# Kernel optimization log

Measured on AMD Instinct MI355X. Metric: run time of the kernel, lower is better.

## Reference

```python
import jax, jax.numpy as jnp
import numpy as np

NUM_PREFIXES = 64  # == head_dim in this config


def setup_inputs() -> dict:
    key = jax.random.key(0)
    ks = jax.random.split(key, 12)
    B, S, H = 2, 2048, 1024
    hd = NUM_PREFIXES
    nh = H // hd              # 16 heads
    din = dout = 128
    kg = H // dout            # key conv groups = 8
    P = S + hd                # position_dim = 2112
    f = jnp.float32
    sc = 0.02
    hidden = jax.random.normal(ks[0], (B, S, H), f)
    # one-hot positions: prefix tokens (first hd) use slots [S, S+hd), rest use their index
    idx = jnp.where(jnp.arange(S) < hd, S + jnp.arange(S), jnp.arange(S))
    pos = jnp.broadcast_to(jax.nn.one_hot(idx, P, dtype=f)[None], (B, S, P))
    mask = jnp.ones((B, 1, S, S), f)  # peak_into_future=True -> full visibility
    return {
        "hidden_states": hidden,
        "position_embeddings": pos,
        "attention_mask": mask,
        "Wq_head": sc * jax.random.normal(ks[1], (hd, nh, nh), f),
        "Wk_group": sc * jax.random.normal(ks[2], (kg, din, din), f),
        "Wk_head": sc * jax.random.normal(ks[3], (dout, kg, kg), f),
        "Wv_head": sc * jax.random.normal(ks[4], (hd, nh, nh), f),
        "p_attn": sc * jax.random.normal(ks[5], (3 * hd, P), f),
        "p_expand": sc * jax.random.normal(ks[6], (3, 1, nh), f),
        "Wc": sc * jax.random.normal(ks[7], (hd, nh, nh), f),
        "Wg": sc * jax.random.normal(ks[8], (2, H), f),
        "Ug": sc * jax.random.normal(ks[9], (2, H), f),
        "Vg": sc * jax.random.normal(ks[10], (2, P), f),
        "bg": jnp.zeros((2,), f),
    }


def reference(hidden_states, position_embeddings, attention_mask,
              Wq_head, Wk_group, Wk_head, Wv_head,
              p_attn, p_expand, Wc, Wg, Ug, Vg, bg):
    B, S, H = hidden_states.shape
    hd, nh, _ = Wq_head.shape
    kg, din, _ = Wk_group.shape
    npf = NUM_PREFIXES
    # LinearDescent.forward: zero out prefix-prefix attention block
    mask = attention_mask.at[:, :, :npf, :npf].set(0.0)
    # --- Attention: conv2d/per-dim head-mixing projections (proj_conv2d, proj_transpose) ---
    xh = hidden_states.reshape(B, S, nh, hd)
    q = jnp.einsum('bshd,dhg->bsgd', xh, Wq_head)      # per-dim mixing across heads
    v = jnp.einsum('bshd,dhg->bsgd', xh, Wv_head)
    # key path: per-group linear (kg groups of din), then per-dim mixing across groups
    xg = hidden_states.reshape(B, S, kg, din)
    k1 = jnp.einsum('bsgd,gde->bsge', xg, Wk_group)
    k2 = jnp.einsum('bsgd,dgh->bshd', k1, Wk_head)     # (B,S,kg,dout)
    k = k2.reshape(B, S, nh, hd)
    # positional q/k/v via p_attn (3*hd x P) + per-head expansion via p_expand (3,1,nh)
    pqkv = jnp.einsum('bsp,cp->bsc', position_embeddings, p_attn).reshape(B, S, 3, hd)
    q = q + p_expand[0, 0][None, None, :, None] * pqkv[:, :, 0][:, :, None, :]
    k = k + p_expand[1, 0][None, None, :, None] * pqkv[:, :, 1][:, :, None, :]
    v = v + p_expand[2, 0][None, None, :, None] * pqkv[:, :, 2][:, :, None, :]
    # linear (non-softmax) attention with multiplicative mask, no causal mask
    scores = jnp.einsum('bqhd,bkhd->bhqk', q, k) * mask
    ctx = jnp.einsum('bhqk,bkhd->bqhd', scores, v)
    out = jnp.einsum('bqhd,dhg->bqgd', ctx, Wc).reshape(B, S, H)
    # --- Gates: two sigmoid gates from hidden, attention output, and positions ---
    g = jax.nn.sigmoid(hidden_states @ Wg.T + out @ Ug.T + position_embeddings @ Vg.T + bg)
    return g[..., 0:1] * out + g[..., 1:2] * hidden_states
```

## Files before the change

### kernel.cpp

```cpp
#include <hip/hip_runtime.h>
#include <math.h>

#define SS   2048
#define PP   2112
#define C3   192
#define NZCAP 16

__device__ __forceinline__ void fma4s(float4& a, float s, const float4& b) {
    a.x += s*b.x; a.y += s*b.y; a.z += s*b.z; a.w += s*b.w;
}
__device__ __forceinline__ void fme4(float4& a, const float4& x, const float4& w) {
    a.x += x.x*w.x; a.y += x.y*w.y; a.z += x.z*w.z; a.w += x.w*w.w;
}
__device__ __forceinline__ float comp(const float4& v, int j) {
    return j==0 ? v.x : j==1 ? v.y : j==2 ? v.z : v.w;
}

__global__ __launch_bounds__(256) void k0_prep(
    const float* __restrict__ Wq, const float* __restrict__ Wv,
    const float* __restrict__ Wc, const float* __restrict__ Wkh,
    const float* __restrict__ Wkg, const float* __restrict__ p_attn,
    float* __restrict__ WqT, float* __restrict__ WvT, float* __restrict__ WcT,
    float* __restrict__ WkhT, float* __restrict__ WkgT, float* __restrict__ pT)
{
    const int t = threadIdx.x, blk = blockIdx.x;
    if (blk < 48) {
        const float* src = (blk < 16) ? Wq : (blk < 32) ? Wv : Wc;
        float* dst = (blk < 16) ? WqT : (blk < 32) ? WvT : WcT;
        int base = (blk & 15) * 1024;
        #pragma unroll
        for (int i = 0; i < 4; ++i) {
            int didx = base + i*256 + t;
            int d = didx & 63, g = (didx>>6)&15, h = didx>>10;
            dst[didx] = src[(d<<8)+(h<<4)+g];
        }
    } else if (blk < 56) {
        int base = (blk-48)*1024;
        #pragma unroll
        for (int i = 0; i < 4; ++i) {
            int didx = base + i*256 + t;
            int dk = didx&127, hk = (didx>>7)&7, g = didx>>10;
            WkhT[didx] = Wkh[dk*64 + g*8 + hk];
        }
    } else if (blk < 184) {
        int base = (blk-56)*1024;
        #pragma unroll
        for (int i = 0; i < 4; ++i) {
            int didx = base + i*256 + t;
            int e = didx&127, g = (didx>>7)&7, d = didx>>10;
            WkgT[didx] = Wkg[(g*128+d)*128 + e];
        }
    } else {
        int base = (blk-184)*1024;
        #pragma unroll
        for (int i = 0; i < 4; ++i) {
            int sidx = base + i*256 + t;
            int c = sidx / PP, p = sidx - c*PP;
            pT[p*C3 + c] = p_attn[sidx];
        }
    }
}

__global__ __launch_bounds__(256) void ka_proj(
    const float* __restrict__ hidden, const float* __restrict__ pos,
    const float* __restrict__ WkgT, const float* __restrict__ WkhT,
    const float* __restrict__ WvT,  const float* __restrict__ pT,
    const float* __restrict__ p_exp, const float* __restrict__ Vg,
    float* __restrict__ ko, float* __restrict__ vo,
    float* __restrict__ pq0, float* __restrict__ posg)
{
    __shared__ __align__(16) float xs[8][1024];
    __shared__ __align__(16) float k1s[8][1024];
    __shared__ __align__(16) float pq[8][C3+4];
    __shared__ int   cnt[8];
    __shared__ int   plist[8][NZCAP];
    __shared__ float vlist[8][NZCAP];

    const int t = threadIdx.x;
    const int row0 = blockIdx.x * 8;

    #pragma unroll
    for (int i = 0; i < 8; ++i)
        ((float4*)xs)[i*256+t] = ((const float4*)hidden)[(size_t)row0*256 + i*256 + t];
    for (int i = t; i < 8*(C3+4); i += 256) ((float*)pq)[i] = 0.f;
    if (t < 8) cnt[t] = 0;
    __syncthreads();

    #pragma unroll
    for (int r = 0; r < 8; ++r) {
        const float4* prow4 = (const float4*)(pos + (size_t)(row0+r)*PP);
        #pragma unroll
        for (int c = 0; c < 3; ++c) {
            int fi = c*256 + t;
            if (fi < PP/4) {
                float4 v4 = prow4[fi];
                float vals[4] = {v4.x, v4.y, v4.z, v4.w};
                #pragma unroll
                for (int u = 0; u < 4; ++u) if (vals[u] != 0.f) {
                    int idx = atomicAdd(&cnt[r], 1);
                    if (idx < NZCAP) { plist[r][idx] = fi*4+u; vlist[r][idx] = vals[u]; }
                    else {
                        int p = fi*4+u; float val = vals[u];
                        for (int cc = 0; cc < C3; ++cc)
                            atomicAdd(&pq[r][cc], val * pT[p*C3+cc]);
                        atomicAdd(&pq[r][C3],   val * Vg[p]);
                        atomicAdd(&pq[r][C3+1], val * Vg[PP+p]);
                    }
                }
            }
        }
    }
    __syncthreads();

    #pragma unroll
    for (int r = 0; r < 8; ++r) {
        int n = min(cnt[r], NZCAP);
        for (int i = 0; i < n; ++i) {
            int p = plist[r][i]; float val = vlist[r][i];
            if (t < C3)           pq[r][t]    += val * pT[p*C3 + t];
            else if (t == C3)     pq[r][C3]   += val * Vg[p];
            else if (t == C3+1)   pq[r][C3+1] += val * Vg[PP+p];
        }
    }
    __syncthreads();

    {
        const int g = t>>4, dq = t&15;
        const float4* WvT4 = (const float4*)WvT;
        const float pev = p_exp[32+g];
        #pragma unroll
        for (int r = 0; r < 8; ++r) {
            float4 av = {0,0,0,0};
            #pragma unroll
            for (int h = 0; h < 16; ++h)
                fme4(av, ((const float4*)xs[r])[h*16+dq], WvT4[(h*16+g)*16+dq]);
            fma4s(av, pev, ((const float4*)&pq[r][128])[dq]);
            ((float4*)vo)[(size_t)(row0+r)*256 + g*16 + dq] = av;
        }
    }

    {
        const int g8 = t>>5, eq = t&31;
        const float4* WkgT4 = (const float4*)WkgT;
        float4 a1[8] = {};
        for (int dq = 0; dq < 32; ++dq) {
            float4 xq[8];
            #pragma unroll
            for (int r = 0; r < 8; ++r) xq[r] = ((const float4*)xs[r])[g8*32 + dq];
            #pragma unroll
            for (int j = 0; j < 4; ++j) {
                int d = dq*4 + j;
                float4 w = WkgT4[(d*8+g8)*32 + eq];
                #pragma unroll
                for (int r = 0; r < 8; ++r) fma4s(a1[r], comp(xq[r], j), w);
            }
        }
        #pragma unroll
        for (int r = 0; r < 8; ++r) ((float4*)k1s[r])[g8*32 + eq] = a1[r];
    }
    __syncthreads();

    {
        const int hk = t>>5, dkq = t&31;
        const int hh = hk*2 + (dkq>>4);
        const float pe = p_exp[16 + hh];
        const float4* WkhT4 = (const float4*)WkhT;
        float4 acc[8] = {};
        #pragma unroll
        for (int g = 0; g < 8; ++g) {
            float4 w = WkhT4[(g*8+hk)*32 + dkq];
            #pragma unroll
            for (int r = 0; r < 8; ++r)
                fme4(acc[r], ((const float4*)k1s[r])[g*32 + dkq], w);
        }
        #pragma unroll
        for (int r = 0; r < 8; ++r) {
            fma4s(acc[r], pe, ((const float4*)&pq[r][64])[dkq&15]);
            ((float4*)ko)[(size_t)(row0+r)*256 + hk*32 + dkq] = acc[r];
        }
    }

    #pragma unroll
    for (int i = 0; i < 2; ++i) {
        int idx = i*256 + t;
        pq0[(size_t)(row0 + (idx>>6))*64 + (idx&63)] = pq[idx>>6][idx&63];
    }
    if (t < 16) posg[(size_t)(row0 + (t>>1))*2 + (t&1)] = pq[t>>1][C3 + (t&1)];
}

__global__ __launch_bounds__(256) void km_kv(
    const float* __restrict__ k, const float* __restrict__ v,
    float* __restrict__ Mpart, float* __restrict__ Mpref)
{
    __shared__ __align__(16) float kt[2048];
    __shared__ __align__(16) float vt[2048];
    const int t  = threadIdx.x;
    const int c  = blockIdx.x >> 5;
    const int bh = blockIdx.x & 31;
    const int b  = bh >> 4, h = bh & 15;
    const int et = t>>4, dt = t&15;
    float acc[4][4]  = {};
    float accp[4][4] = {};

    #pragma unroll
    for (int tile = 0; tile < 4; ++tile) {
        const int r0 = c*128 + tile*32;
        #pragma unroll
        for (int i = 0; i < 2; ++i) {
            int fi = t + 256*i;
            int r = fi>>4, q4 = fi&15;
            size_t ga = (size_t)(b*SS + r0 + r)*256 + h*16 + q4;
            ((float4*)kt)[fi] = ((const float4*)k)[ga];
            ((float4*)vt)[fi] = ((const float4*)v)[ga];
        }
        __syncthreads();
        const bool pf = (c==0) && (tile<2);
        #pragma unroll 4
        for (int r = 0; r < 32; ++r) {
            float4 kk = ((const float4*)kt)[r*16+et];
            float4 vv = ((const float4*)vt)[r*16+dt];
            float ka[4]={kk.x,kk.y,kk.z,kk.w}, va[4]={vv.x,vv.y,vv.z,vv.w};
            #pragma unroll
            for (int i2=0;i2<4;++i2)
                #pragma unroll
                for (int j=0;j<4;++j) acc[i2][j] += ka[i2]*va[j];
            if (pf) {
                #pragma unroll
                for (int i2=0;i2<4;++i2)
                    #pragma unroll
                    for (int j=0;j<4;++j) accp[i2][j] += ka[i2]*va[j];
            }
        }
        __syncthreads();
    }
    float4* Mc = (float4*)(Mpart + ((size_t)c*32 + bh)*4096);
    #pragma unroll
    for (int i2=0;i2<4;++i2) {
        float4 o = {acc[i2][0],acc[i2][1],acc[i2][2],acc[i2][3]};
        Mc[(et*4+i2)*16 + dt] = o;
    }
    if (c == 0) {
        float4* Mp = (float4*)(Mpref + (size_t)bh*4096);
        #pragma unroll
        for (int i2=0;i2<4;++i2) {
            float4 o = {accp[i2][0],accp[i2][1],accp[i2][2],accp[i2][3]};
            Mp[(et*4+i2)*16 + dt] = o;
        }
    }
}

__global__ __launch_bounds__(256) void kr_red(
    const float* __restrict__ Mpart, float* __restrict__ Mfull)
{
    int qid = blockIdx.x*256 + threadIdx.x;
    float4 s = {0,0,0,0};
    #pragma unroll
    for (int c = 0; c < 16; ++c) {
        float4 m = ((const float4*)Mpart)[(size_t)c*32768 + qid];
        s.x+=m.x; s.y+=m.y; s.z+=m.z; s.w+=m.w;
    }
    ((float4*)Mfull)[qid] = s;
}

__global__ __launch_bounds__(256) void kb_out(
    const float* __restrict__ hidden, const float* __restrict__ pq0,
    const float* __restrict__ posg,   const float* __restrict__ Mfull,
    const float* __restrict__ Mpref,  const float* __restrict__ WqT,
    const float* __restrict__ p_exp,  const float* __restrict__ WcT,
    const float* __restrict__ Wg,     const float* __restrict__ Ug,
    const float* __restrict__ bg,     float* __restrict__ yo)
{
    __shared__ __align__(16) float xs[8][1024];
    __shared__ __align__(16) float qs[8][1024];
    __shared__ __align__(16) float pq0s[8][64];
    __shared__ float gs[32];
    const int t  = threadIdx.x;
    const int b  = blockIdx.x >> 8;
    const int s0 = (blockIdx.x & 255) * 8;
    const size_t rqbase = ((size_t)b*SS + s0) * 256;

    float4 xv[8];
    #pragma unroll
    for (int r = 0; r < 8; ++r) {
        xv[r] = ((const float4*)hidden)[rqbase + r*256 + t];
        ((float4*)xs[r])[t] = xv[r];
    }
    if (t < 128) ((float4*)pq0s)[t] = ((const float4*)pq0)[((size_t)b*SS + s0)*16 + t];
    if (t < 32) gs[t] = 0.f;
    __syncthreads();

    float pW0[8], pW1[8];
    {
        float4 w0 = ((const float4*)Wg)[t], w1 = ((const float4*)Wg)[256+t];
        #pragma unroll
        for (int r = 0; r < 8; ++r) {
            pW0[r] = xv[r].x*w0.x + xv[r].y*w0.y + xv[r].z*w0.z + xv[r].w*w0.w;
            pW1[r] = xv[r].x*w1.x + xv[r].y*w1.y + xv[r].z*w1.z + xv[r].w*w1.w;
        }
    }

    const int g = t>>4, dq = t&15;
    {
        const float4* WqT4 = (const float4*)WqT;
        const float peq = p_exp[g];
        #pragma unroll
        for (int r = 0; r < 8; ++r) {
            float4 aq = {0,0,0,0};
            #pragma unroll
            for (int h = 0; h < 16; ++h)
                fme4(aq, ((const float4*)xs[r])[h*16+dq], WqT4[(h*16+g)*16+dq]);
            fma4s(aq, peq, ((const float4*)pq0s[r])[dq]);
            ((float4*)qs[r])[g*16+dq] = aq;
        }
    }
    __syncthreads();

    {
        const float4* Mf4 = (const float4*)Mfull + ((size_t)b*16 + g)*1024;
        const float4* Mp4 = (const float4*)Mpref + ((size_t)b*16 + g)*1024;
        const bool pf = (s0 < 64);
        float4 acc[8] = {};
        for (int eq = 0; eq < 16; ++eq) {
            float4 qq[8];
            #pragma unroll
            for (int r = 0; r < 8; ++r) qq[r] = ((const float4*)qs[r])[g*16 + eq];
            #pragma unroll
            for (int j = 0; j < 4; ++j) {
                int e = eq*4 + j;
                float4 m = Mf4[e*16 + dq];
                if (pf) { float4 mp = Mp4[e*16+dq]; m.x-=mp.x; m.y-=mp.y; m.z-=mp.z; m.w-=mp.w; }
                #pragma unroll
                for (int r = 0; r < 8; ++r) fma4s(acc[r], comp(qq[r],j), m);
            }
        }
        #pragma unroll
        for (int r = 0; r < 8; ++r) ((float4*)xs[r])[g*16 + dq] = acc[r];
    }
    __syncthreads();

    float pU0[8], pU1[8];
    {
        const float4* WcT4 = (const float4*)WcT;
        float4 u0 = ((const float4*)Ug)[g*16+dq], u1 = ((const float4*)Ug)[256 + g*16+dq];
        #pragma unroll
        for (int r = 0; r < 8; ++r) {
            float4 o = {0,0,0,0};
            #pragma unroll
            for (int h = 0; h < 16; ++h)
                fme4(o, ((const float4*)xs[r])[h*16+dq], WcT4[(h*16+g)*16+dq]);
            ((float4*)qs[r])[g*16+dq] = o;
            pU0[r] = o.x*u0.x + o.y*u0.y + o.z*u0.z + o.w*u0.w;
            pU1[r] = o.x*u1.x + o.y*u1.y + o.z*u1.z + o.w*u1.w;
        }
    }

    #pragma unroll
    for (int r = 0; r < 8; ++r) {
        float v0 = pW0[r], v1 = pW1[r], v2 = pU0[r], v3 = pU1[r];
        #pragma unroll
        for (int off = 32; off > 0; off >>= 1) {
            v0 += __shfl_down(v0, off);
            v1 += __shfl_down(v1, off);
            v2 += __shfl_down(v2, off);
            v3 += __shfl_down(v3, off);
        }
        if ((t & 63) == 0) {
            atomicAdd(&gs[r*4+0], v0);
            atomicAdd(&gs[r*4+1], v1);
            atomicAdd(&gs[r*4+2], v2);
            atomicAdd(&gs[r*4+3], v3);
        }
    }
    __syncthreads();

    #pragma unroll
    for (int r = 0; r < 8; ++r) {
        size_t grow = (size_t)b*SS + s0 + r;
        float z0 = gs[r*4+0] + gs[r*4+2] + posg[grow*2+0] + bg[0];
        float z1 = gs[r*4+1] + gs[r*4+3] + posg[grow*2+1] + bg[1];
        float G0 = 1.f/(1.f+expf(-z0));
        float G1 = 1.f/(1.f+expf(-z1));
        float4 o = ((const float4*)qs[r])[t];
        float4 y;
        y.x = G0*o.x + G1*xv[r].x;
        y.y = G0*o.y + G1*xv[r].y;
        y.z = G0*o.z + G1*xv[r].z;
        y.w = G0*o.w + G1*xv[r].w;
        ((float4*)yo)[rqbase + r*256 + t] = y;
    }
}

extern "C" void kernel_launch(void* const* d_in, const int* in_sizes, int n_in,
                              void* d_out, int out_size, void* d_ws, size_t ws_size,
                              hipStream_t stream)
{
    const float* hidden = (const float*)d_in[0];
    const float* pos    = (const float*)d_in[1];
    const float* Wq     = (const float*)d_in[3];
    const float* Wkg    = (const float*)d_in[4];
    const float* Wkh    = (const float*)d_in[5];
    const float* Wv     = (const float*)d_in[6];
    const float* p_attn = (const float*)d_in[7];
    const float* p_exp  = (const float*)d_in[8];
    const float* Wc     = (const float*)d_in[9];
    const float* Wg     = (const float*)d_in[10];
    const float* Ug     = (const float*)d_in[11];
    const float* Vg     = (const float*)d_in[12];
    const float* bg     = (const float*)d_in[13];

    float* ws    = (float*)d_ws;
    float* ko    = ws;
    float* vo    = ws + 4194304;
    float* Mpart = ws + 8388608;
    float* Mpref = ws + 10485760;
    float* Mfull = ws + 10616832;
    float* pq0   = ws + 10747904;
    float* posg  = ws + 11010048;
    float* WqT   = ws + 11018240;
    float* WvT   = ws + 11034624;
    float* WcT   = ws + 11051008;
    float* WkhT  = ws + 11067392;
    float* WkgT  = ws + 11075584;
    float* pT    = ws + 11206656;

    k0_prep<<<dim3(580), dim3(256), 0, stream>>>(Wq, Wv, Wc, Wkh, Wkg, p_attn,
                                                 WqT, WvT, WcT, WkhT, WkgT, pT);
    ka_proj<<<dim3(512), dim3(256), 0, stream>>>(hidden, pos, WkgT, WkhT, WvT, pT,
                                                 p_exp, Vg, ko, vo, pq0, posg);
    km_kv<<<dim3(512), dim3(256), 0, stream>>>(ko, vo, Mpart, Mpref);
    kr_red<<<dim3(128), dim3(256), 0, stream>>>(Mpart, Mfull);
    kb_out<<<dim3(512), dim3(256), 0, stream>>>(hidden, pq0, posg, Mfull, Mpref,
                                                WqT, p_exp, WcT, Wg, Ug, bg, (float*)d_out);
}
```

Measured before the change: 270.1 us.

## Double threads per block in projection/output kernels and split KV chunks finer

```diff
diff --git a/kernel.cpp b/kernel.cpp
--- a/kernel.cpp
+++ b/kernel.cpp
@@ -14,6 +14,9 @@
 }
 __device__ __forceinline__ float comp(const float4& v, int j) {
     return j==0 ? v.x : j==1 ? v.y : j==2 ? v.z : v.w;
+}
+__device__ __forceinline__ float dot4(const float4& a, const float4& b) {
+    return a.x*b.x + a.y*b.y + a.z*b.z + a.w*b.w;
 }
 
 __global__ __launch_bounds__(256) void k0_prep(
@@ -61,7 +64,7 @@
     }
 }
 
-__global__ __launch_bounds__(256) void ka_proj(
+__global__ __launch_bounds__(512) void ka_proj(
     const float* __restrict__ hidden, const float* __restrict__ pos,
     const float* __restrict__ WkgT, const float* __restrict__ WkhT,
     const float* __restrict__ WvT,  const float* __restrict__ pT,
@@ -70,7 +73,6 @@
     float* __restrict__ pq0, float* __restrict__ posg)
 {
     __shared__ __align__(16) float xs[8][1024];
-    __shared__ __align__(16) float k1s[8][1024];
     __shared__ __align__(16) float pq[8][C3+4];
     __shared__ int   cnt[8];
     __shared__ int   plist[8][NZCAP];
@@ -80,9 +82,9 @@
     const int row0 = blockIdx.x * 8;
 
     #pragma unroll
-    for (int i = 0; i < 8; ++i)
-        ((float4*)xs)[i*256+t] = ((const float4*)hidden)[(size_t)row0*256 + i*256 + t];
-    for (int i = t; i < 8*(C3+4); i += 256) ((float*)pq)[i] = 0.f;
+    for (int i = 0; i < 4; ++i)
+        ((float4*)xs)[i*512+t] = ((const float4*)hidden)[(size_t)row0*256 + i*512 + t];
+    for (int i = t; i < 8*(C3+4); i += 512) ((float*)pq)[i] = 0.f;
     if (t < 8) cnt[t] = 0;
     __syncthreads();
 
@@ -90,8 +92,8 @@
     for (int r = 0; r < 8; ++r) {
         const float4* prow4 = (const float4*)(pos + (size_t)(row0+r)*PP);
         #pragma unroll
-        for (int c = 0; c < 3; ++c) {
-            int fi = c*256 + t;
+        for (int c = 0; c < 2; ++c) {
+            int fi = c*512 + t;
             if (fi < PP/4) {
                 float4 v4 = prow4[fi];
                 float vals[4] = {v4.x, v4.y, v4.z, v4.w};
@@ -125,11 +127,12 @@
     __syncthreads();
 
     {
-        const int g = t>>4, dq = t&15;
+        const int rh = t>>8, g = (t>>4)&15, dq = t&15;
         const float4* WvT4 = (const float4*)WvT;
         const float pev = p_exp[32+g];
         #pragma unroll
-        for (int r = 0; r < 8; ++r) {
+        for (int rr = 0; rr < 4; ++rr) {
+            int r = rh*4+rr;
             float4 av = {0,0,0,0};
             #pragma unroll
             for (int h = 0; h < 16; ++h)
@@ -139,52 +142,55 @@
         }
     }
 
-    {
-        const int g8 = t>>5, eq = t&31;
+    float4 a1[4] = {};
+    {
+        const int g8 = t>>6, rh = (t>>5)&1, eq = t&31;
         const float4* WkgT4 = (const float4*)WkgT;
-        float4 a1[8] = {};
         for (int dq = 0; dq < 32; ++dq) {
-            float4 xq[8];
-            #pragma unroll
-            for (int r = 0; r < 8; ++r) xq[r] = ((const float4*)xs[r])[g8*32 + dq];
+            float4 xq[4];
+            #pragma unroll
+            for (int rr = 0; rr < 4; ++rr)
+                xq[rr] = ((const float4*)xs[rh*4+rr])[g8*32 + dq];
             #pragma unroll
             for (int j = 0; j < 4; ++j) {
                 int d = dq*4 + j;
                 float4 w = WkgT4[(d*8+g8)*32 + eq];
                 #pragma unroll
-                for (int r = 0; r < 8; ++r) fma4s(a1[r], comp(xq[r], j), w);
+                for (int rr = 0; rr < 4; ++rr) fma4s(a1[rr], comp(xq[rr], j), w);
             }
         }
-        #pragma unroll
-        for (int r = 0; r < 8; ++r) ((float4*)k1s[r])[g8*32 + eq] = a1[r];
-    }
-    __syncthreads();
-
-    {
-        const int hk = t>>5, dkq = t&31;
+    }
+    __syncthreads();
+    {
+        const int g8 = t>>6, rh = (t>>5)&1, eq = t&31;
+        #pragma unroll
+        for (int rr = 0; rr < 4; ++rr)
+            ((float4*)xs[rh*4+rr])[g8*32 + eq] = a1[rr];
+    }
+    __syncthreads();
+
+    {
+        const int hk = t>>6, rh = (t>>5)&1, dkq = t&31;
         const int hh = hk*2 + (dkq>>4);
         const float pe = p_exp[16 + hh];
         const float4* WkhT4 = (const float4*)WkhT;
-        float4 acc[8] = {};
+        float4 acc[4] = {};
         #pragma unroll
         for (int g = 0; g < 8; ++g) {
             float4 w = WkhT4[(g*8+hk)*32 + dkq];
             #pragma unroll
-            for (int r = 0; r < 8; ++r)
-                fme4(acc[r], ((const float4*)k1s[r])[g*32 + dkq], w);
-        }
-        #pragma unroll
-        for (int r = 0; r < 8; ++r) {
-            fma4s(acc[r], pe, ((const float4*)&pq[r][64])[dkq&15]);
-            ((float4*)ko)[(size_t)(row0+r)*256 + hk*32 + dkq] = acc[r];
-        }
-    }
-
-    #pragma unroll
-    for (int i = 0; i < 2; ++i) {
-        int idx = i*256 + t;
-        pq0[(size_t)(row0 + (idx>>6))*64 + (idx&63)] = pq[idx>>6][idx&63];
-    }
+            for (int rr = 0; rr < 4; ++rr)
+                fme4(acc[rr], ((const float4*)xs[rh*4+rr])[g*32 + dkq], w);
+        }
+        #pragma unroll
+        for (int rr = 0; rr < 4; ++rr) {
+            int r = rh*4+rr;
+            fma4s(acc[rr], pe, ((const float4*)&pq[r][64])[dkq&15]);
+            ((float4*)ko)[(size_t)(row0+r)*256 + hk*32 + dkq] = acc[rr];
+        }
+    }
+
+    pq0[(size_t)(row0 + (t>>6))*64 + (t&63)] = pq[t>>6][t&63];
     if (t < 16) posg[(size_t)(row0 + (t>>1))*2 + (t&1)] = pq[t>>1][C3 + (t&1)];
 }
 
@@ -199,12 +205,13 @@
     const int bh = blockIdx.x & 31;
     const int b  = bh >> 4, h = bh & 15;
     const int et = t>>4, dt = t&15;
+    const bool pf = (c == 0);
     float acc[4][4]  = {};
     float accp[4][4] = {};
 
     #pragma unroll
-    for (int tile = 0; tile < 4; ++tile) {
-        const int r0 = c*128 + tile*32;
+    for (int tile = 0; tile < 2; ++tile) {
+        const int r0 = c*64 + tile*32;
         #pragma unroll
         for (int i = 0; i < 2; ++i) {
             int fi = t + 256*i;
@@ -214,7 +221,6 @@
             ((float4*)vt)[fi] = ((const float4*)v)[ga];
         }
         __syncthreads();
-        const bool pf = (c==0) && (tile<2);
         #pragma unroll 4
         for (int r = 0; r < 32; ++r) {
             float4 kk = ((const float4*)kt)[r*16+et];
@@ -239,7 +245,7 @@
         float4 o = {acc[i2][0],acc[i2][1],acc[i2][2],acc[i2][3]};
         Mc[(et*4+i2)*16 + dt] = o;
     }
-    if (c == 0) {
+    if (pf) {
         float4* Mp = (float4*)(Mpref + (size_t)bh*4096);
         #pragma unroll
         for (int i2=0;i2<4;++i2) {
@@ -253,16 +259,17 @@
     const float* __restrict__ Mpart, float* __restrict__ Mfull)
 {
     int qid = blockIdx.x*256 + threadIdx.x;
+    int bh = qid >> 10, inner = qid & 1023;
     float4 s = {0,0,0,0};
     #pragma unroll
-    for (int c = 0; c < 16; ++c) {
-        float4 m = ((const float4*)Mpart)[(size_t)c*32768 + qid];
+    for (int c = 0; c < 32; ++c) {
+        float4 m = ((const float4*)Mpart)[(((size_t)c*32 + bh)<<10) + inner];
         s.x+=m.x; s.y+=m.y; s.z+=m.z; s.w+=m.w;
     }
     ((float4*)Mfull)[qid] = s;
 }
 
-__global__ __launch_bounds__(256) void kb_out(
+__global__ __launch_bounds__(512) void kb_out(
     const float* __restrict__ hidden, const float* __restrict__ pq0,
     const float* __restrict__ posg,   const float* __restrict__ Mfull,
     const float* __restrict__ Mpref,  const float* __restrict__ WqT,
@@ -279,38 +286,38 @@
     const int s0 = (blockIdx.x & 255) * 8;
     const size_t rqbase = ((size_t)b*SS + s0) * 256;
 
-    float4 xv[8];
-    #pragma unroll
-    for (int r = 0; r < 8; ++r) {
-        xv[r] = ((const float4*)hidden)[rqbase + r*256 + t];
-        ((float4*)xs[r])[t] = xv[r];
-    }
+    #pragma unroll
+    for (int i = 0; i < 4; ++i)
+        ((float4*)xs)[i*512+t] = ((const float4*)hidden)[rqbase + i*512 + t];
     if (t < 128) ((float4*)pq0s)[t] = ((const float4*)pq0)[((size_t)b*SS + s0)*16 + t];
     if (t < 32) gs[t] = 0.f;
     __syncthreads();
 
-    float pW0[8], pW1[8];
-    {
-        float4 w0 = ((const float4*)Wg)[t], w1 = ((const float4*)Wg)[256+t];
-        #pragma unroll
-        for (int r = 0; r < 8; ++r) {
-            pW0[r] = xv[r].x*w0.x + xv[r].y*w0.y + xv[r].z*w0.z + xv[r].w*w0.w;
-            pW1[r] = xv[r].x*w1.x + xv[r].y*w1.y + xv[r].z*w1.z + xv[r].w*w1.w;
-        }
-    }
-
-    const int g = t>>4, dq = t&15;
+    const int rh = t>>8, c = t&255, g = c>>4, dq = c&15;
+
+    float4 xv[4]; float pW0[4], pW1[4];
+    {
+        float4 w0 = ((const float4*)Wg)[c], w1 = ((const float4*)Wg)[256+c];
+        #pragma unroll
+        for (int rr = 0; rr < 4; ++rr) {
+            xv[rr] = ((const float4*)xs[rh*4+rr])[c];
+            pW0[rr] = dot4(xv[rr], w0);
+            pW1[rr] = dot4(xv[rr], w1);
+        }
+    }
+
     {
         const float4* WqT4 = (const float4*)WqT;
         const float peq = p_exp[g];
         #pragma unroll
-        for (int r = 0; r < 8; ++r) {
+        for (int rr = 0; rr < 4; ++rr) {
+            int row = rh*4+rr;
             float4 aq = {0,0,0,0};
             #pragma unroll
             for (int h = 0; h < 16; ++h)
-                fme4(aq, ((const float4*)xs[r])[h*16+dq], WqT4[(h*16+g)*16+dq]);
-            fma4s(aq, peq, ((const float4*)pq0s[r])[dq]);
-            ((float4*)qs[r])[g*16+dq] = aq;
+                fme4(aq, ((const float4*)xs[row])[h*16+dq], WqT4[(h*16+g)*16+dq]);
+            fma4s(aq, peq, ((const float4*)pq0s[row])[dq]);
+            ((float4*)qs[row])[c] = aq;
         }
     }
     __syncthreads();
@@ -319,44 +326,48 @@
         const float4* Mf4 = (const float4*)Mfull + ((size_t)b*16 + g)*1024;
         const float4* Mp4 = (const float4*)Mpref + ((size_t)b*16 + g)*1024;
         const bool pf = (s0 < 64);
-        float4 acc[8] = {};
+        float4 acc[4] = {};
         for (int eq = 0; eq < 16; ++eq) {
-            float4 qq[8];
-            #pragma unroll
-            for (int r = 0; r < 8; ++r) qq[r] = ((const float4*)qs[r])[g*16 + eq];
+            float4 qq[4];
+            #pragma unroll
+            for (int rr = 0; rr < 4; ++rr)
+                qq[rr] = ((const float4*)qs[rh*4+rr])[g*16 + eq];
             #pragma unroll
             for (int j = 0; j < 4; ++j) {
-                int e = eq*4 + j;
-                float4 m = Mf4[e*16 + dq];
-                if (pf) { float4 mp = Mp4[e*16+dq]; m.x-=mp.x; m.y-=mp.y; m.z-=mp.z; m.w-=mp.w; }
+                float4 m = Mf4[(eq*4+j)*16 + dq];
+                if (pf) { float4 mp = Mp4[(eq*4+j)*16+dq];
+                          m.x-=mp.x; m.y-=mp.y; m.z-=mp.z; m.w-=mp.w; }
                 #pragma unroll
-                for (int r = 0; r < 8; ++r) fma4s(acc[r], comp(qq[r],j), m);
+                for (int rr = 0; rr < 4; ++rr) fma4s(acc[rr], comp(qq[rr],j), m);
             }
         }
-        #pragma unroll
-        for (int r = 0; r < 8; ++r) ((float4*)xs[r])[g*16 + dq] = acc[r];
-    }
-    __syncthreads();
-
-    float pU0[8], pU1[8];
+        __syncthreads();
+        #pragma unroll
+        for (int rr = 0; rr < 4; ++rr) ((float4*)xs[rh*4+rr])[c] = acc[rr];
+    }
+    __syncthreads();
+
+    float4 oo[4]; float pU0[4], pU1[4];
     {
         const float4* WcT4 = (const float4*)WcT;
-        float4 u0 = ((const float4*)Ug)[g*16+dq], u1 = ((const float4*)Ug)[256 + g*16+dq];
-        #pragma unroll
-        for (int r = 0; r < 8; ++r) {
+        float4 u0 = ((const float4*)Ug)[c], u1 = ((const float4*)Ug)[256+c];
+        #pragma unroll
+        for (int rr = 0; rr < 4; ++rr) {
+            int row = rh*4+rr;
             float4 o = {0,0,0,0};
             #pragma unroll
             for (int h = 0; h < 16; ++h)
-                fme4(o, ((const float4*)xs[r])[h*16+dq], WcT4[(h*16+g)*16+dq]);
-            ((float4*)qs[r])[g*16+dq] = o;
-            pU0[r] = o.x*u0.x + o.y*u0.y + o.z*u0.z + o.w*u0.w;
-            pU1[r] = o.x*u1.x + o.y*u1.y + o.z*u1.z + o.w*u1.w;
-        }
-    }
-
-    #pragma unroll
-    for (int r = 0; r < 8; ++r) {
-        float v0 = pW0[r], v1 = pW1[r], v2 = pU0[r], v3 = pU1[r];
+                fme4(o, ((const float4*)xs[row])[h*16+dq], WcT4[(h*16+g)*16+dq]);
+            oo[rr] = o;
+            pU0[rr] = dot4(o, u0);
+            pU1[rr] = dot4(o, u1);
+        }
+    }
+
+    #pragma unroll
+    for (int rr = 0; rr < 4; ++rr) {
+        int row = rh*4+rr;
+        float v0 = pW0[rr], v1 = pW1[rr], v2 = pU0[rr], v3 = pU1[rr];
         #pragma unroll
         for (int off = 32; off > 0; off >>= 1) {
             v0 += __shfl_down(v0, off);
@@ -365,28 +376,28 @@
             v3 += __shfl_down(v3, off);
         }
         if ((t & 63) == 0) {
-            atomicAdd(&gs[r*4+0], v0);
-            atomicAdd(&gs[r*4+1], v1);
-            atomicAdd(&gs[r*4+2], v2);
-            atomicAdd(&gs[r*4+3], v3);
-        }
-    }
-    __syncthreads();
-
-    #pragma unroll
-    for (int r = 0; r < 8; ++r) {
-        size_t grow = (size_t)b*SS + s0 + r;
-        float z0 = gs[r*4+0] + gs[r*4+2] + posg[grow*2+0] + bg[0];
-        float z1 = gs[r*4+1] + gs[r*4+3] + posg[grow*2+1] + bg[1];
+            atomicAdd(&gs[row*4+0], v0);
+            atomicAdd(&gs[row*4+1], v1);
+            atomicAdd(&gs[row*4+2], v2);
+            atomicAdd(&gs[row*4+3], v3);
+        }
+    }
+    __syncthreads();
+
+    #pragma unroll
+    for (int rr = 0; rr < 4; ++rr) {
+        int row = rh*4+rr;
+        size_t grow = (size_t)b*SS + s0 + row;
+        float z0 = gs[row*4+0] + gs[row*4+2] + posg[grow*2+0] + bg[0];
+        float z1 = gs[row*4+1] + gs[row*4+3] + posg[grow*2+1] + bg[1];
         float G0 = 1.f/(1.f+expf(-z0));
         float G1 = 1.f/(1.f+expf(-z1));
-        float4 o = ((const float4*)qs[r])[t];
         float4 y;
-        y.x = G0*o.x + G1*xv[r].x;
-        y.y = G0*o.y + G1*xv[r].y;
-        y.z = G0*o.z + G1*xv[r].z;
-        y.w = G0*o.w + G1*xv[r].w;
-        ((float4*)yo)[rqbase + r*256 + t] = y;
+        y.x = G0*oo[rr].x + G1*xv[rr].x;
+        y.y = G0*oo[rr].y + G1*xv[rr].y;
+        y.z = G0*oo[rr].z + G1*xv[rr].z;
+        y.w = G0*oo[rr].w + G1*xv[rr].w;
+        ((float4*)yo)[rqbase + row*256 + c] = y;
     }
 }
 
@@ -412,23 +423,23 @@
     float* ko    = ws;
     float* vo    = ws + 4194304;
     float* Mpart = ws + 8388608;
-    float* Mpref = ws + 10485760;
-    float* Mfull = ws + 10616832;
-    float* pq0   = ws + 10747904;
-    float* posg  = ws + 11010048;
-    float* WqT   = ws + 11018240;
-    float* WvT   = ws + 11034624;
-    float* WcT   = ws + 11051008;
-    float* WkhT  = ws + 11067392;
-    float* WkgT  = ws + 11075584;
-    float* pT    = ws + 11206656;
+    float* Mpref = ws + 12582912;
+    float* Mfull = ws + 12713984;
+    float* pq0   = ws + 12845056;
+    float* posg  = ws + 13107200;
+    float* WqT   = ws + 13115392;
+    float* WvT   = ws + 13131776;
+    float* WcT   = ws + 13148160;
+    float* WkhT  = ws + 13164544;
+    float* WkgT  = ws + 13172736;
+    float* pT    = ws + 13303808;
 
     k0_prep<<<dim3(580), dim3(256), 0, stream>>>(Wq, Wv, Wc, Wkh, Wkg, p_attn,
                                                  WqT, WvT, WcT, WkhT, WkgT, pT);
-    ka_proj<<<dim3(512), dim3(256), 0, stream>>>(hidden, pos, WkgT, WkhT, WvT, pT,
+    ka_proj<<<dim3(512), dim3(512), 0, stream>>>(hidden, pos, WkgT, WkhT, WvT, pT,
                                                  p_exp, Vg, ko, vo, pq0, posg);
-    km_kv<<<dim3(512), dim3(256), 0, stream>>>(ko, vo, Mpart, Mpref);
+    km_kv<<<dim3(1024), dim3(256), 0, stream>>>(ko, vo, Mpart, Mpref);
     kr_red<<<dim3(128), dim3(256), 0, stream>>>(Mpart, Mfull);
-    kb_out<<<dim3(512), dim3(256), 0, stream>>>(hidden, pq0, posg, Mfull, Mpref,
+    kb_out<<<dim3(512), dim3(512), 0, stream>>>(hidden, pq0, posg, Mfull, Mpref,
                                                 WqT, p_exp, WcT, Wg, Ug, bg, (float*)d_out);
 }
```

New measurement: 379.8 us. 1.41x slower.
